# Optimization experiments

Measured on AMD Instinct MI355X. Metric: run time of the kernel, lower is better.

## Reference

```python
import jax, jax.numpy as jnp
import numpy as np

BATCH = 4096
IN_SIZES = [1024, 1024, 1024, 1024]
EMB = 2048  # embracement_size


def setup_inputs() -> dict:
    key = jax.random.key(0)
    keys = jax.random.split(key, 3 * len(IN_SIZES))
    inp = {}
    for i, d in enumerate(IN_SIZES):
        inp[f"x{i}"] = jax.random.normal(keys[3 * i], (BATCH, d), dtype=jnp.float32)
        # Linear params (Kaiming-ish scale)
        inp[f"W{i}"] = jax.random.normal(keys[3 * i + 1], (d, EMB), dtype=jnp.float32) / np.sqrt(d)
        inp[f"b{i}"] = jax.random.normal(keys[3 * i + 2], (EMB,), dtype=jnp.float32) * 0.01
    return inp


def _sample_indices(batch, num_feats, emb):
    # availabilities=None, selection_probabilities=None -> uniform p over modalities
    # multinomial(p, num_samples=emb, replacement=True) == categorical over log p
    logits = jnp.zeros((batch, num_feats), dtype=jnp.float32)  # uniform
    k = jax.random.key(42)
    # shape (emb, batch) broadcasts against logits batch shape (batch,)
    idx = jax.random.categorical(k, logits, axis=-1, shape=(emb, batch))
    return idx.T  # [batch, emb]


def reference(x0, W0, b0, x1, W1, b1, x2, W2, b2, x3, W3, b3):
    xs = [x0, x1, x2, x3]
    Ws = [W0, W1, W2, W3]
    bs = [b0, b1, b2, b3]
    # docking: Linear + ReLU per modality -> [batch, EMB, num_feats]
    dock = jnp.stack([jax.nn.relu(x @ W + b) for x, W, b in zip(xs, Ws, bs)], axis=-1)
    B, E, F = dock.shape
    idx = _sample_indices(B, F, E)  # [B, E] int32
    # gather along modality axis (replaces one-hot multiply-sum)
    out = jnp.take_along_axis(dock, idx[:, :, None], axis=-1)[..., 0]
    return out  # [batch, EMB]
```

## Files before the change

### kernel.cpp

```cpp
#include <hip/hip_runtime.h>
#include <stdint.h>


typedef short short8 __attribute__((ext_vector_type(8)));
typedef float floatx4 __attribute__((ext_vector_type(4)));

#define B_DIM 4096
#define K_DIM 1024
#define E_DIM 2048

__device__ __forceinline__ uint16_t f2bf(float x) {
  uint32_t u = __float_as_uint(x);
  u += 0x7FFFu + ((u >> 16) & 1u);
  return (uint16_t)(u >> 16);
}

__device__ __forceinline__ void threefry(uint32_t x0, uint32_t x1,
                                         uint32_t& o0, uint32_t& o1) {
  const uint32_t ks0 = 0u;
  const uint32_t ks1 = 42u;
  const uint32_t ks2 = 0x1BD11BDAu ^ 42u;
  x0 += ks0; x1 += ks1;
#define TF_R(r) { x0 += x1; x1 = (x1 << r) | (x1 >> (32 - r)); x1 ^= x0; }
  TF_R(13) TF_R(15) TF_R(26) TF_R(6)
  x0 += ks1; x1 += ks2 + 1u;
  TF_R(17) TF_R(29) TF_R(16) TF_R(24)
  x0 += ks2; x1 += ks0 + 2u;
  TF_R(13) TF_R(15) TF_R(26) TF_R(6)
  x0 += ks0; x1 += ks1 + 3u;
  TF_R(17) TF_R(29) TF_R(16) TF_R(24)
  x0 += ks1; x1 += ks2 + 4u;
  TF_R(13) TF_R(15) TF_R(26) TF_R(6)
  x0 += ks2; x1 += ks0 + 5u;
#undef TF_R
  o0 = x0; o1 = x1;
}

__global__ __launch_bounds__(256) void idx_kernel(uint32_t* __restrict__ idx2) {
  uint32_t tid = blockIdx.x * 256u + threadIdx.x;
  uint32_t base = tid << 6;
  uint32_t word = 0;
#pragma unroll 2
  for (int j = 0; j < 16; ++j) {
    uint32_t c = base + 4u * j;
    uint32_t best = 0, bi = 0;
#pragma unroll
    for (uint32_t f = 0; f < 4; ++f) {
      uint32_t y0, y1;
      threefry(0u, c + f, y0, y1);
      uint32_t m = (y0 ^ y1) >> 9;
      if (f == 0) best = m;
      else if (m > best) { best = m; bi = f; }
    }
    word |= bi << (2 * j);
  }
  idx2[tid] = word;
}

__global__ __launch_bounds__(256) void convert_x(
    const float* __restrict__ x0, const float* __restrict__ x1,
    const float* __restrict__ x2, const float* __restrict__ x3,
    uint16_t* __restrict__ xb) {
  int f = blockIdx.z;
  const float* x = (f == 0) ? x0 : (f == 1) ? x1 : (f == 2) ? x2 : x3;
  size_t i = ((size_t)blockIdx.x * 256 + threadIdx.x) * 4;
  float4 v = *(const float4*)(x + i);
  union { uint16_t h[4]; uint64_t q; } p;
  p.h[0] = f2bf(v.x); p.h[1] = f2bf(v.y);
  p.h[2] = f2bf(v.z); p.h[3] = f2bf(v.w);
  *(uint64_t*)(xb + (size_t)f * B_DIM * K_DIM + i) = p.q;
}

__global__ __launch_bounds__(256) void convert_w(
    const float* __restrict__ W0, const float* __restrict__ W1,
    const float* __restrict__ W2, const float* __restrict__ W3,
    uint16_t* __restrict__ Wt) {
  __shared__ float tile[32][33];
  int f = blockIdx.z;
  const float* W = (f == 0) ? W0 : (f == 1) ? W1 : (f == 2) ? W2 : W3;
  int e0 = blockIdx.x * 32, k0 = blockIdx.y * 32;
  int tx = threadIdx.x, ty = threadIdx.y;
#pragma unroll
  for (int i = 0; i < 4; ++i)
    tile[ty + i * 8][tx] = W[(size_t)(k0 + ty + i * 8) * E_DIM + e0 + tx];
  __syncthreads();
  uint16_t* dst = Wt + (size_t)f * E_DIM * K_DIM;
#pragma unroll
  for (int i = 0; i < 4; ++i)
    dst[(size_t)(e0 + ty + i * 8) * K_DIM + k0 + tx] = f2bf(tile[tx][ty + i * 8]);
}

__device__ __forceinline__ void async16(const uint16_t* g, uint16_t* lds) {
  __builtin_amdgcn_global_load_lds(
      (const __attribute__((address_space(1))) void*)g,
      (__attribute__((address_space(3))) void*)lds, 16, 0, 0);
}

__global__ __launch_bounds__(256, 2) void gemm_fused(
    const uint16_t* __restrict__ Ab, const uint16_t* __restrict__ Bbt,
    const uint32_t* __restrict__ idx2,
    const float* __restrict__ bias0, const float* __restrict__ bias1,
    const float* __restrict__ bias2, const float* __restrict__ bias3,
    float* __restrict__ out) {
  __shared__ uint16_t As[128 * 32];
  __shared__ uint16_t Bs[128 * 32];

  const int tid = threadIdx.x;
  const int w = tid >> 6;
  const int l = tid & 63;
  const int mBase = blockIdx.y * 128;
  const int nBase = blockIdx.x * 128;

  const int wm = (w >> 1) * 64, wn = (w & 1) * 64;
  const int ar = l >> 2, ac8 = l & 3;
  const int fr = l & 15, fq = l >> 4;

  const int b_hi0 = (mBase + wm) >> 4;
  uint32_t iw[4][4];
#pragma unroll
  for (int ni = 0; ni < 4; ++ni) {
    int col = nBase + wn + ni * 16 + fr;
#pragma unroll
    for (int mi = 0; mi < 4; ++mi)
      iw[ni][mi] = idx2[(size_t)col * (B_DIM / 16) + b_hi0 + mi];
  }

  floatx4 res[4][4] = {};

#pragma unroll 1
  for (int f = 0; f < 4; ++f) {
    const uint16_t* A = Ab  + (size_t)f * B_DIM * K_DIM + (size_t)mBase * K_DIM;
    const uint16_t* B = Bbt + (size_t)f * E_DIM * K_DIM + (size_t)nBase * K_DIM;

    floatx4 acc[4][4] = {};
    for (int k0 = 0; k0 < K_DIM; k0 += 32) {
      #pragma unroll
      for (int t = 0; t < 2; ++t) {
        int c = w * 2 + t;
        async16(A + (size_t)(c * 16 + ar) * K_DIM + k0 + ac8 * 8, &As[c * 512]);
        async16(B + (size_t)(c * 16 + ar) * K_DIM + k0 + ac8 * 8, &Bs[c * 512]);
      }
      __syncthreads();

      short8 a[4], b[4];
      #pragma unroll
      for (int mi = 0; mi < 4; ++mi)
        a[mi] = *(const short8*)&As[(wm + mi * 16 + fr) * 32 + fq * 8];
      #pragma unroll
      for (int ni = 0; ni < 4; ++ni)
        b[ni] = *(const short8*)&Bs[(wn + ni * 16 + fr) * 32 + fq * 8];
      #pragma unroll
      for (int mi = 0; mi < 4; ++mi)
        #pragma unroll
        for (int ni = 0; ni < 4; ++ni)
          acc[mi][ni] = __builtin_amdgcn_mfma_f32_16x16x32_bf16(
              a[mi], b[ni], acc[mi][ni], 0, 0, 0);
      __syncthreads();
    }

    const float* bias = (f == 0) ? bias0 : (f == 1) ? bias1
                      : (f == 2) ? bias2 : bias3;
    #pragma unroll
    for (int ni = 0; ni < 4; ++ni) {
      float bvf = bias[nBase + wn + ni * 16 + fr];
      #pragma unroll
      for (int mi = 0; mi < 4; ++mi) {
        uint32_t wd = iw[ni][mi];
        #pragma unroll
        for (int r = 0; r < 4; ++r) {
          uint32_t sel = (wd >> (2 * (fq * 4 + r))) & 3u;
          if (sel == (uint32_t)f) res[mi][ni][r] = acc[mi][ni][r] + bvf;
        }
      }
    }
  }

#pragma unroll
  for (int ni = 0; ni < 4; ++ni) {
    int col = nBase + wn + ni * 16 + fr;
#pragma unroll
    for (int mi = 0; mi < 4; ++mi) {
      int row0 = mBase + wm + mi * 16 + fq * 4;
#pragma unroll
      for (int r = 0; r < 4; ++r) {
        float o = res[mi][ni][r];
        __builtin_nontemporal_store(o > 0.f ? o : 0.f,
                                    &out[(size_t)(row0 + r) * E_DIM + col]);
      }
    }
  }
}

extern "C" void kernel_launch(void* const* d_in, const int* in_sizes, int n_in,
                              void* d_out, int out_size, void* d_ws, size_t ws_size,
                              hipStream_t stream) {
  const float* x[4]; const float* W[4]; const float* bs[4];
  for (int f = 0; f < 4; ++f) {
    x[f]  = (const float*)d_in[3 * f + 0];
    W[f]  = (const float*)d_in[3 * f + 1];
    bs[f] = (const float*)d_in[3 * f + 2];
  }
  char* ws = (char*)d_ws;
  uint16_t* xb  = (uint16_t*)ws;
  uint16_t* Wt  = (uint16_t*)(ws + (size_t)32 * 1024 * 1024);
  uint32_t* idx2 = (uint32_t*)(ws + (size_t)48 * 1024 * 1024);
  float* out = (float*)d_out;

  idx_kernel<<<dim3(2048), dim3(256), 0, stream>>>(idx2);
  convert_x<<<dim3(4096, 1, 4), dim3(256), 0, stream>>>(x[0], x[1], x[2], x[3], xb);
  convert_w<<<dim3(64, 32, 4), dim3(32, 8), 0, stream>>>(W[0], W[1], W[2], W[3], Wt);
  gemm_fused<<<dim3(E_DIM / 128, B_DIM / 128), dim3(256), 0, stream>>>(
      xb, Wt, idx2, bs[0], bs[1], bs[2], bs[3], out);
}
```

Before: 309.2 us.

## Fuse prep kernels and double-buffer GEMM with swizzled 64-wide K tiles

Merges the index-generation, x conversion and W transpose kernels into one prep kernel, writing the indices byte-wise and using alignbit for the rotates. The GEMM now stages 64-wide K tiles into double-buffered LDS with an XOR swizzle, prefetching the next tile while computing on the current one and keeping a single barrier per step. This aims to cut launch overhead and hide global-load latency and LDS bank conflicts. In exchange it quadruples LDS use per block, which may lower occupancy.

```diff
diff --git a/kernel.cpp b/kernel.cpp
--- a/kernel.cpp
+++ b/kernel.cpp
@@ -8,6 +8,10 @@
 #define B_DIM 4096
 #define K_DIM 1024
 #define E_DIM 2048
+
+__device__ __forceinline__ uint32_t rotl32(uint32_t x, uint32_t r) {
+  return __builtin_amdgcn_alignbit(x, x, 32u - r);
+}
 
 __device__ __forceinline__ uint16_t f2bf(float x) {
   uint32_t u = __float_as_uint(x);
@@ -21,7 +25,7 @@
   const uint32_t ks1 = 42u;
   const uint32_t ks2 = 0x1BD11BDAu ^ 42u;
   x0 += ks0; x1 += ks1;
-#define TF_R(r) { x0 += x1; x1 = (x1 << r) | (x1 >> (32 - r)); x1 ^= x0; }
+#define TF_R(r) { x0 += x1; x1 = rotl32(x1, r); x1 ^= x0; }
   TF_R(13) TF_R(15) TF_R(26) TF_R(6)
   x0 += ks1; x1 += ks2 + 1u;
   TF_R(17) TF_R(29) TF_R(16) TF_R(24)
@@ -36,58 +40,71 @@
   o0 = x0; o1 = x1;
 }
 
-__global__ __launch_bounds__(256) void idx_kernel(uint32_t* __restrict__ idx2) {
-  uint32_t tid = blockIdx.x * 256u + threadIdx.x;
-  uint32_t base = tid << 6;
-  uint32_t word = 0;
-#pragma unroll 2
-  for (int j = 0; j < 16; ++j) {
-    uint32_t c = base + 4u * j;
-    uint32_t best = 0, bi = 0;
-#pragma unroll
-    for (uint32_t f = 0; f < 4; ++f) {
-      uint32_t y0, y1;
-      threefry(0u, c + f, y0, y1);
-      uint32_t m = (y0 ^ y1) >> 9;
-      if (f == 0) best = m;
-      else if (m > best) { best = m; bi = f; }
-    }
-    word |= bi << (2 * j);
-  }
-  idx2[tid] = word;
-}
-
-__global__ __launch_bounds__(256) void convert_x(
+__global__ __launch_bounds__(256) void prep_kernel(
     const float* __restrict__ x0, const float* __restrict__ x1,
     const float* __restrict__ x2, const float* __restrict__ x3,
-    uint16_t* __restrict__ xb) {
-  int f = blockIdx.z;
-  const float* x = (f == 0) ? x0 : (f == 1) ? x1 : (f == 2) ? x2 : x3;
-  size_t i = ((size_t)blockIdx.x * 256 + threadIdx.x) * 4;
-  float4 v = *(const float4*)(x + i);
-  union { uint16_t h[4]; uint64_t q; } p;
-  p.h[0] = f2bf(v.x); p.h[1] = f2bf(v.y);
-  p.h[2] = f2bf(v.z); p.h[3] = f2bf(v.w);
-  *(uint64_t*)(xb + (size_t)f * B_DIM * K_DIM + i) = p.q;
-}
-
-__global__ __launch_bounds__(256) void convert_w(
     const float* __restrict__ W0, const float* __restrict__ W1,
     const float* __restrict__ W2, const float* __restrict__ W3,
-    uint16_t* __restrict__ Wt) {
+    uint16_t* __restrict__ xb, uint16_t* __restrict__ Wt,
+    uint8_t* __restrict__ idx1) {
   __shared__ float tile[32][33];
-  int f = blockIdx.z;
+  const uint32_t g = blockIdx.x;
+  const int t = threadIdx.x;
+  const int f = g >> 11;
+  const uint32_t ip = g & 2047u;
+
+  const float* x = (f == 0) ? x0 : (f == 1) ? x1 : (f == 2) ? x2 : x3;
+  const size_t xoff = ((size_t)ip * 256 + t) * 8;
+  float4 v0 = *(const float4*)(x + xoff);
+  float4 v1 = *(const float4*)(x + xoff + 4);
+
   const float* W = (f == 0) ? W0 : (f == 1) ? W1 : (f == 2) ? W2 : W3;
-  int e0 = blockIdx.x * 32, k0 = blockIdx.y * 32;
-  int tx = threadIdx.x, ty = threadIdx.y;
+  const int e0 = (int)(ip & 63) * 32, k0 = (int)(ip >> 6) * 32;
+  const int tx = t & 31, ty = t >> 5;
+  float wv[4];
 #pragma unroll
   for (int i = 0; i < 4; ++i)
-    tile[ty + i * 8][tx] = W[(size_t)(k0 + ty + i * 8) * E_DIM + e0 + tx];
+    wv[i] = W[(size_t)(k0 + ty + i * 8) * E_DIM + e0 + tx];
+
+  const uint32_t o0i = (g * 256u + t) * 4u;
+  uint32_t byte = 0;
+#pragma unroll
+  for (uint32_t q = 0; q < 4; ++q) {
+    uint32_t c = (o0i + q) << 2;
+    uint32_t best = 0, bi = 0;
+#pragma unroll
+    for (uint32_t ff = 0; ff < 4; ++ff) {
+      uint32_t y0, y1;
+      threefry(0u, c + ff, y0, y1);
+      uint32_t m = (y0 ^ y1) >> 9;
+      if (ff == 0) best = m;
+      else if (m > best) { best = m; bi = ff; }
+    }
+    byte |= bi << (2 * q);
+  }
+  idx1[g * 256u + t] = (uint8_t)byte;
+
+  {
+    union { uint16_t h[8]; uint64_t q[2]; } p;
+    p.h[0] = f2bf(v0.x); p.h[1] = f2bf(v0.y);
+    p.h[2] = f2bf(v0.z); p.h[3] = f2bf(v0.w);
+    p.h[4] = f2bf(v1.x); p.h[5] = f2bf(v1.y);
+    p.h[6] = f2bf(v1.z); p.h[7] = f2bf(v1.w);
+    uint64_t* dst = (uint64_t*)(xb + (size_t)f * B_DIM * K_DIM + xoff);
+    dst[0] = p.q[0]; dst[1] = p.q[1];
+  }
+
+#pragma unroll
+  for (int i = 0; i < 4; ++i) tile[ty + i * 8][tx] = wv[i];
   __syncthreads();
-  uint16_t* dst = Wt + (size_t)f * E_DIM * K_DIM;
-#pragma unroll
-  for (int i = 0; i < 4; ++i)
-    dst[(size_t)(e0 + ty + i * 8) * K_DIM + k0 + tx] = f2bf(tile[tx][ty + i * 8]);
+  {
+    const int el = t >> 3, kc = (t & 7) * 4;
+    union { uint16_t h[4]; uint64_t q; } p;
+#pragma unroll
+    for (int i = 0; i < 4; ++i) p.h[i] = f2bf(tile[kc + i][el]);
+    uint16_t* dst = Wt + (size_t)f * E_DIM * K_DIM;
+    *(uint64_t*)(dst + (size_t)(e0 + el) * K_DIM + k0 + kc) = p.q;
+  }
 }
 
 __device__ __forceinline__ void async16(const uint16_t* g, uint16_t* lds) {
@@ -102,8 +119,8 @@
     const float* __restrict__ bias0, const float* __restrict__ bias1,
     const float* __restrict__ bias2, const float* __restrict__ bias3,
     float* __restrict__ out) {
-  __shared__ uint16_t As[128 * 32];
-  __shared__ uint16_t Bs[128 * 32];
+  __shared__ uint16_t As[2][128 * 64];
+  __shared__ uint16_t Bs[2][128 * 64];
 
   const int tid = threadIdx.x;
   const int w = tid >> 6;
@@ -112,7 +129,8 @@
   const int nBase = blockIdx.x * 128;
 
   const int wm = (w >> 1) * 64, wn = (w & 1) * 64;
-  const int ar = l >> 2, ac8 = l & 3;
+  const int sr = l >> 3;
+  const int skc = ((l & 7) ^ sr) * 8;
   const int fr = l & 15, fq = l >> 4;
 
   const int b_hi0 = (mBase + wm) >> 4;
@@ -131,42 +149,63 @@
   for (int f = 0; f < 4; ++f) {
     const uint16_t* A = Ab  + (size_t)f * B_DIM * K_DIM + (size_t)mBase * K_DIM;
     const uint16_t* B = Bbt + (size_t)f * E_DIM * K_DIM + (size_t)nBase * K_DIM;
+    const uint16_t* Aw = A + (size_t)(32 * w + sr) * K_DIM + skc;
+    const uint16_t* Bw = B + (size_t)(32 * w + sr) * K_DIM + skc;
 
     floatx4 acc[4][4] = {};
-    for (int k0 = 0; k0 < K_DIM; k0 += 32) {
-      #pragma unroll
-      for (int t = 0; t < 2; ++t) {
-        int c = w * 2 + t;
-        async16(A + (size_t)(c * 16 + ar) * K_DIM + k0 + ac8 * 8, &As[c * 512]);
-        async16(B + (size_t)(c * 16 + ar) * K_DIM + k0 + ac8 * 8, &Bs[c * 512]);
+
+#pragma unroll
+    for (int tt = 0; tt < 4; ++tt) {
+      async16(Aw + (size_t)(8 * tt) * K_DIM, &As[0][(4 * w + tt) * 512]);
+      async16(Bw + (size_t)(8 * tt) * K_DIM, &Bs[0][(4 * w + tt) * 512]);
+    }
+    __syncthreads();
+
+    int buf = 0;
+#pragma unroll 1
+    for (int kt = 0; kt < 16; ++kt) {
+      int kn = (kt + 1) * 64;
+      if (kt + 1 < 16) {
+#pragma unroll
+        for (int tt = 0; tt < 4; ++tt) {
+          async16(Aw + (size_t)(8 * tt) * K_DIM + kn, &As[buf ^ 1][(4 * w + tt) * 512]);
+          async16(Bw + (size_t)(8 * tt) * K_DIM + kn, &Bs[buf ^ 1][(4 * w + tt) * 512]);
+        }
+      }
+#pragma unroll
+      for (int h = 0; h < 2; ++h) {
+        short8 a[4], b[4];
+        const int ch = h * 4 + fq;
+#pragma unroll
+        for (int mi = 0; mi < 4; ++mi) {
+          int row = wm + mi * 16 + fr;
+          a[mi] = *(const short8*)&As[buf][row * 64 + (ch ^ (fr & 7)) * 8];
+        }
+#pragma unroll
+        for (int ni = 0; ni < 4; ++ni) {
+          int row = wn + ni * 16 + fr;
+          b[ni] = *(const short8*)&Bs[buf][row * 64 + (ch ^ (fr & 7)) * 8];
+        }
+#pragma unroll
+        for (int mi = 0; mi < 4; ++mi)
+#pragma unroll
+          for (int ni = 0; ni < 4; ++ni)
+            acc[mi][ni] = __builtin_amdgcn_mfma_f32_16x16x32_bf16(
+                a[mi], b[ni], acc[mi][ni], 0, 0, 0);
       }
       __syncthreads();
-
-      short8 a[4], b[4];
-      #pragma unroll
-      for (int mi = 0; mi < 4; ++mi)
-        a[mi] = *(const short8*)&As[(wm + mi * 16 + fr) * 32 + fq * 8];
-      #pragma unroll
-      for (int ni = 0; ni < 4; ++ni)
-        b[ni] = *(const short8*)&Bs[(wn + ni * 16 + fr) * 32 + fq * 8];
-      #pragma unroll
-      for (int mi = 0; mi < 4; ++mi)
-        #pragma unroll
-        for (int ni = 0; ni < 4; ++ni)
-          acc[mi][ni] = __builtin_amdgcn_mfma_f32_16x16x32_bf16(
-              a[mi], b[ni], acc[mi][ni], 0, 0, 0);
-      __syncthreads();
+      buf ^= 1;
     }
 
     const float* bias = (f == 0) ? bias0 : (f == 1) ? bias1
                       : (f == 2) ? bias2 : bias3;
-    #pragma unroll
+#pragma unroll
     for (int ni = 0; ni < 4; ++ni) {
       float bvf = bias[nBase + wn + ni * 16 + fr];
-      #pragma unroll
+#pragma unroll
       for (int mi = 0; mi < 4; ++mi) {
         uint32_t wd = iw[ni][mi];
-        #pragma unroll
+#pragma unroll
         for (int r = 0; r < 4; ++r) {
           uint32_t sel = (wd >> (2 * (fq * 4 + r))) & 3u;
           if (sel == (uint32_t)f) res[mi][ni][r] = acc[mi][ni][r] + bvf;
@@ -203,12 +242,11 @@
   char* ws = (char*)d_ws;
   uint16_t* xb  = (uint16_t*)ws;
   uint16_t* Wt  = (uint16_t*)(ws + (size_t)32 * 1024 * 1024);
-  uint32_t* idx2 = (uint32_t*)(ws + (size_t)48 * 1024 * 1024);
+  uint8_t*  idx1 = (uint8_t*)(ws + (size_t)48 * 1024 * 1024);
   float* out = (float*)d_out;
 
-  idx_kernel<<<dim3(2048), dim3(256), 0, stream>>>(idx2);
-  convert_x<<<dim3(4096, 1, 4), dim3(256), 0, stream>>>(x[0], x[1], x[2], x[3], xb);
-  convert_w<<<dim3(64, 32, 4), dim3(32, 8), 0, stream>>>(W[0], W[1], W[2], W[3], Wt);
+  prep_kernel<<<dim3(8192), dim3(256), 0, stream>>>(
+      x[0], x[1], x[2], x[3], W[0], W[1], W[2], W[3], xb, Wt, idx1);
   gemm_fused<<<dim3(E_DIM / 128, B_DIM / 128), dim3(256), 0, stream>>>(
-      xb, Wt, idx2, bs[0], bs[1], bs[2], bs[3], out);
-}
+      xb, Wt, (const uint32_t*)idx1, bs[0], bs[1], bs[2], bs[3], out);
+}
```

Result: faster. 254.2 us (-17.8%).
